# Optimization experiments

Measured on AMD Instinct MI355X. Metric: run time of the kernel, lower is better.

The kernel has to match this reference:

```python
import jax, jax.numpy as jnp
import numpy as np
import math

HEAD_DIM = 128
NUM_Q_HEAD = 32
NUM_KV_HEAD = 8
WINDOW = 512
CAP = 30.0
CLIP_LO, CLIP_HI = -0.03, 1.03
EPS = 1e-5
SCALE = 1.0 / math.sqrt(HEAD_DIM)
B, S = 2, 2048


def group_rms_norm(x, w, group_size, eps):
    # x: [B, S, hidden]; normalize each contiguous group of size group_size
    Bx, Sx, H = x.shape
    ng = H // group_size
    xg = x.reshape(Bx, Sx, ng, group_size)
    inv = jax.lax.rsqrt(jnp.mean(xg * xg, axis=-1, keepdims=True) + eps)
    return (xg * inv).reshape(Bx, Sx, H) * w


def setup_inputs() -> dict:
    key = jax.random.key(0)
    kq, kk, kv, kw1, kw2 = jax.random.split(key, 5)
    q = jax.random.normal(kq, (B, S, NUM_Q_HEAD, HEAD_DIM), dtype=jnp.float32)
    k = jax.random.normal(kk, (B, S, NUM_KV_HEAD, HEAD_DIM), dtype=jnp.float32)
    v = jax.random.normal(kv, (B, S, NUM_KV_HEAD, HEAD_DIM), dtype=jnp.float32)
    # GroupRMSNorm weights, init uniform in (-1, 1)
    q_norm_w = jax.random.uniform(kw1, (NUM_Q_HEAD * HEAD_DIM,), dtype=jnp.float32, minval=-1.0, maxval=1.0)
    kv_norm_w = jax.random.uniform(kw2, (NUM_KV_HEAD * HEAD_DIM,), dtype=jnp.float32, minval=-1.0, maxval=1.0)
    return {"q": q, "k": k, "v": v, "q_norm_w": q_norm_w, "kv_norm_w": kv_norm_w}


def reference(q, k, v, q_norm_w, kv_norm_w):
    Bq, Sq, Hq, D = q.shape
    Sk = k.shape[1]
    # QK GroupRMSNorm over flattened hidden dim, group_size = head_dim
    qn = group_rms_norm(q.reshape(Bq, Sq, Hq * D), q_norm_w, HEAD_DIM, EPS).reshape(q.shape)
    kn = group_rms_norm(k.reshape(Bq, Sk, NUM_KV_HEAD * D), kv_norm_w, HEAD_DIM, EPS).reshape(k.shape)
    # GQA: repeat_interleave kv heads along head axis
    rep = Hq // NUM_KV_HEAD
    kr = jnp.repeat(kn, rep, axis=2)  # [B, Sk, Hq, D]
    vr = jnp.repeat(v, rep, axis=2)
    # scores: [B, Hq, Sq, Sk]
    scores = jnp.einsum("bqhd,bkhd->bhqk", qn, kr) * SCALE
    scores = CAP * jnp.tanh(scores / CAP)  # softmax capping
    # sliding-window + causal mask: allowed iff i - WINDOW <= j <= i (offset = Sk - Sq = 0)
    offset = Sk - Sq
    i = jnp.arange(Sq)[:, None] + offset
    j = jnp.arange(Sk)[None, :]
    allowed = (j <= i) & (j >= i - WINDOW)
    scores = jnp.where(allowed, scores, -jnp.inf)
    probs = jax.nn.softmax(scores, axis=-1)
    probs = jnp.nan_to_num(probs, nan=0.0)
    # softmax clipping
    probs = jnp.clip((CLIP_HI - CLIP_LO) * probs + CLIP_LO, 0.0, 1.0)
    out = jnp.einsum("bhqk,bkhd->bqhd", probs, vr)
    return out
```

## Files before the change

### kernel.cpp

```cpp
#include <hip/hip_runtime.h>

#define SEQ 2048
#define DD 128
#define HQ 32
#define HKV 8
#define WIN 512

typedef unsigned short u16;
typedef unsigned int u32;
typedef __attribute__((ext_vector_type(8))) short bf16x8;
typedef __attribute__((ext_vector_type(4))) float f32x4;
typedef __attribute__((ext_vector_type(2))) float f32x2;

#define SBAR() asm volatile("s_barrier" ::: "memory")
#define WAITV0() asm volatile("s_waitcnt vmcnt(0)" ::: "memory")

__device__ __forceinline__ u16 f2bf(float f) {
  u32 u = __builtin_bit_cast(u32, f);
  u += 0x7FFFu + ((u >> 16) & 1u);
  return (u16)(u >> 16);
}

__device__ __forceinline__ void gl16(const void* g, void* l) {
  __builtin_amdgcn_global_load_lds(
      (const __attribute__((address_space(1))) void*)g,
      (__attribute__((address_space(3))) void*)l, 16, 0, 0);
}

__device__ __forceinline__ u32 cvtpk(float lo, float hi) {
  u32 r;
  asm("v_cvt_pk_bf16_f32 %0, %1, %2" : "=v"(r) : "v"(lo), "v"(hi));
  return r;
}

__device__ __forceinline__ f32x2 pk_mul(f32x2 a, f32x2 b) {
  f32x2 d;
  asm("v_pk_mul_f32 %0, %1, %2" : "=v"(d) : "v"(a), "v"(b));
  return d;
}
__device__ __forceinline__ f32x2 pk_fma(f32x2 a, f32x2 b, f32x2 c) {
  f32x2 d;
  asm("v_pk_fma_f32 %0, %1, %2, %3" : "=v"(d) : "v"(a), "v"(b), "v"(c));
  return d;
}
__device__ __forceinline__ f32x2 pk_add(f32x2 a, f32x2 b) {
  f32x2 d;
  asm("v_pk_add_f32 %0, %1, %2" : "=v"(d) : "v"(a), "v"(b));
  return d;
}

__device__ __forceinline__ f32x2 score2(f32x2 x, f32x2 vL2E, f32x2 vmCE, f32x2 vmCTL) {
  f32x2 x2 = pk_mul(x, x);
  f32x2 a1 = pk_fma(x, vL2E, vmCE);
  f32x2 b1 = pk_mul(x2, vmCTL);
  return pk_fma(b1, x, a1);
}

__device__ __forceinline__ f32x2 unpk(u32 wv) {
  f32x2 r;
  r[0] = __builtin_bit_cast(float, wv << 16);
  r[1] = __builtin_bit_cast(float, wv & 0xFFFF0000u);
  return r;
}

__device__ __forceinline__ void norm_body(
    const float* __restrict__ x, const float* __restrict__ w,
    u16* __restrict__ o, int hshift, int blk, int tid) {
  const int lane = tid & 63;
  const int wv = tid >> 6;
  const int sub = lane >> 5;
  const int l5 = lane & 31;
  const int rid = blk * 8 + wv * 2 + sub;
  const int H = 1 << hshift;
  const int hh = rid & (H - 1);
  const int s = (rid >> hshift) & (SEQ - 1);
  const int b = rid >> (hshift + 11);
  const float4 xv = *(reinterpret_cast<const float4*>(x + (size_t)rid * DD) + l5);
  float ssq = xv.x * xv.x + xv.y * xv.y + xv.z * xv.z + xv.w * xv.w;
  ssq += __shfl_xor(ssq, 1);
  ssq += __shfl_xor(ssq, 2);
  ssq += __shfl_xor(ssq, 4);
  ssq += __shfl_xor(ssq, 8);
  ssq += __shfl_xor(ssq, 16);
  const float inv = rsqrtf(ssq * (1.0f / 128.0f) + 1e-5f);
  const float4 wv4 = *(reinterpret_cast<const float4*>(w + hh * DD) + l5);
  const u16 o0 = f2bf(xv.x * inv * wv4.x);
  const u16 o1 = f2bf(xv.y * inv * wv4.y);
  const u16 o2 = f2bf(xv.z * inv * wv4.z);
  const u16 o3 = f2bf(xv.w * inv * wv4.w);
  const size_t oo = (((size_t)b * H + hh) * SEQ + s) * DD + l5 * 4;
  uint2 pk;
  pk.x = (u32)o0 | ((u32)o1 << 16);
  pk.y = (u32)o2 | ((u32)o3 << 16);
  *reinterpret_cast<uint2*>(o + oo) = pk;
}

__device__ __forceinline__ void transv_body(
    const float* __restrict__ v, u16* __restrict__ vt, int bid, int t) {
  const int st = bid & 31;
  const int h = (bid >> 5) & 7;
  const int b = bid >> 8;
  const int sbase = st * 64;
  const int d = t & 127;
  const int sch = (t >> 7) * 32;
  const size_t oo = (((size_t)(b * HKV + h)) * DD + d) * SEQ + sbase + sch;
#pragma unroll
  for (int q8 = 0; q8 < 4; ++q8) {
    uint4 o;
    u32 c[4];
#pragma unroll
    for (int p = 0; p < 4; ++p) {
      const int ss0 = q8 * 8 + p * 2;
      const int s0 = sbase + sch + ss0;
      const float a0 = v[((size_t)(b * SEQ + s0) * HKV + h) * DD + d];
      const float a1 = v[((size_t)(b * SEQ + s0 + 1) * HKV + h) * DD + d];
      c[p] = (u32)f2bf(a0) | ((u32)f2bf(a1) << 16);
    }
    o.x = c[0]; o.y = c[1]; o.z = c[2]; o.w = c[3];
    *reinterpret_cast<uint4*>(vt + oo + q8 * 8) = o;
  }
}

__global__ void __launch_bounds__(256) prep_kernel(
    const float* __restrict__ k, const float* __restrict__ v,
    const float* __restrict__ kw, u16* __restrict__ kn, u16* __restrict__ vt) {
  const int blk = blockIdx.x;
  const int tid = threadIdx.x;
  if (blk < 4096) {
    norm_body(k, kw, kn, 3, blk, tid);
  } else {
    transv_body(v, vt, blk - 4096, tid);
  }
}

__global__ void __launch_bounds__(256, 3) attn_kernel(
    const float* __restrict__ q32, const float* __restrict__ qw,
    const u16* __restrict__ kn, const u16* __restrict__ vt,
    float* __restrict__ out) {
  __shared__ char smem[32768];
  const int tid = threadIdx.x;
  const int w = tid >> 6;
  const int lane = tid & 63;
  const int c = lane & 15;
  const int g = lane >> 4;

  const int p = blockIdx.x;
  const int bid = ((p & 7) << 8) + (p >> 3);
  const int qt = (bid & 127) ^ 127;
  const int hk = (bid >> 7) & 7;
  const int b = bid >> 10;
  const int i0 = qt * 16;
  const int h = hk * 4 + w;

  const u16* kbp = kn + (size_t)(b * HKV + hk) * SEQ * DD;
  const u16* vbp = vt + (size_t)(b * HKV + hk) * DD * SEQ;

  int ks = i0 - WIN;
  ks = (ks < 0) ? 0 : (ks & ~63);
  const int ntl = (i0 + 16 - ks + 63) >> 6;

  auto stageK = [&](int kb, int bufoff) {
    char* dst = smem + bufoff;
#pragma unroll
    for (int ci = 0; ci < 4; ++ci) {
      const int call = w * 4 + ci;
      const int row = call * 4 + g;
      const int ch = c ^ (row & 7);
      gl16(kbp + (size_t)(kb + row) * DD + ch * 8, dst + call * 1024);
    }
  };
  auto stageV = [&](int kb, int bufoff) {
    char* dst = smem + bufoff;
#pragma unroll
    for (int ci = 0; ci < 4; ++ci) {
      const int call = w * 4 + ci;
      const int vrow = call * 8 + (lane >> 3);
      const int vch = (lane & 7) ^ (vrow & 7);
      gl16(vbp + (size_t)vrow * SEQ + kb + vch * 8, dst + call * 1024);
    }
  };

  stageK(ks, 0);

  union AQ { bf16x8 v; u32 w4[4]; };
  AQ aq[4];
  {
    const float* qf = q32 + (((size_t)b * SEQ + i0 + c) * HQ + h) * DD;
    const float* wf = qw + h * DD;
    float xv[4][8];
    float ss = 0.0f;
#pragma unroll
    for (int kt = 0; kt < 4; ++kt) {
      const float4 a0 = *reinterpret_cast<const float4*>(qf + kt * 32 + g * 8);
      const float4 a1 = *reinterpret_cast<const float4*>(qf + kt * 32 + g * 8 + 4);
      xv[kt][0] = a0.x; xv[kt][1] = a0.y; xv[kt][2] = a0.z; xv[kt][3] = a0.w;
      xv[kt][4] = a1.x; xv[kt][5] = a1.y; xv[kt][6] = a1.z; xv[kt][7] = a1.w;
      ss = fmaf(a0.x, a0.x, ss); ss = fmaf(a0.y, a0.y, ss);
      ss = fmaf(a0.z, a0.z, ss); ss = fmaf(a0.w, a0.w, ss);
      ss = fmaf(a1.x, a1.x, ss); ss = fmaf(a1.y, a1.y, ss);
      ss = fmaf(a1.z, a1.z, ss); ss = fmaf(a1.w, a1.w, ss);
    }
    ss += __shfl_xor(ss, 16);
    ss += __shfl_xor(ss, 32);
    const float inv = rsqrtf(ss * (1.0f / 128.0f) + 1e-5f) * 0.08838834764831845f;
#pragma unroll
    for (int kt = 0; kt < 4; ++kt) {
      const float4 w0 = *reinterpret_cast<const float4*>(wf + kt * 32 + g * 8);
      const float4 w1 = *reinterpret_cast<const float4*>(wf + kt * 32 + g * 8 + 4);
      aq[kt].w4[0] = cvtpk(xv[kt][0] * inv * w0.x, xv[kt][1] * inv * w0.y);
      aq[kt].w4[1] = cvtpk(xv[kt][2] * inv * w0.z, xv[kt][3] * inv * w0.w);
      aq[kt].w4[2] = cvtpk(xv[kt][4] * inv * w1.x, xv[kt][5] * inv * w1.y);
      aq[kt].w4[3] = cvtpk(xv[kt][6] * inv * w1.z, xv[kt][7] * inv * w1.w);
    }
  }

  const f32x2 vL2E = {1.44269504088896f, 1.44269504088896f};
  const f32x2 vmCE = {-43.2808512266689f, -43.2808512266689f};
  const f32x2 vmCTL = {-5.343315e-4f, -5.343315e-4f};

  u32 ebuf[9][8];
  f32x2 lsum2 = {0.0f, 0.0f};

#pragma unroll
  for (int t = 0; t < 9; ++t) {
    if (t >= ntl) continue;
    const int kb = ks + t * 64;
    WAITV0();
    SBAR();
    if (t + 1 < ntl) stageK(kb + 64, ((t + 1) & 1) << 14);

    const char* kbuf = smem + ((t & 1) << 14);
    f32x4 sc[4] = {};
    __builtin_amdgcn_s_setprio(1);
#pragma unroll
    for (int nt = 0; nt < 4; ++nt) {
      const int jb = kb + nt * 16;
      if (jb > i0 + 15 || jb + 15 < i0 - WIN) continue;
      const int row = nt * 16 + c;
      const int sw = row & 7;
      const char* base = kbuf + row * 256;
#pragma unroll
      for (int kt = 0; kt < 4; ++kt) {
        const bf16x8 bk = *reinterpret_cast<const bf16x8*>(base + (((kt * 4 + g) ^ sw) << 4));
        sc[nt] = __builtin_amdgcn_mfma_f32_16x16x32_bf16(bk, aq[kt].v, sc[nt], 0, 0, 0);
      }
    }
    __builtin_amdgcn_s_setprio(0);

#pragma unroll
    for (int nt = 0; nt < 4; ++nt) {
      const int jb = kb + nt * 16;
      if (jb > i0 + 15 || jb + 15 < i0 - WIN) {
        ebuf[t][nt * 2] = 0;
        ebuf[t][nt * 2 + 1] = 0;
        continue;
      }
      const bool needmask = (jb + 15 > i0) || (jb < i0 + 15 - WIN);
      f32x2 lo = __builtin_shufflevector(sc[nt], sc[nt], 0, 1);
      f32x2 hi = __builtin_shufflevector(sc[nt], sc[nt], 2, 3);
      const f32x2 a0 = score2(lo, vL2E, vmCE, vmCTL);
      const f32x2 a1 = score2(hi, vL2E, vmCE, vmCTL);
      float e0 = __builtin_amdgcn_exp2f(a0[0]);
      float e1 = __builtin_amdgcn_exp2f(a0[1]);
      float e2 = __builtin_amdgcn_exp2f(a1[0]);
      float e3 = __builtin_amdgcn_exp2f(a1[1]);
      if (needmask) {
        const int difg = i0 + c - jb - g * 4;
        e0 = ((u32)(difg - 0) <= WIN) ? e0 : 0.0f;
        e1 = ((u32)(difg - 1) <= WIN) ? e1 : 0.0f;
        e2 = ((u32)(difg - 2) <= WIN) ? e2 : 0.0f;
        e3 = ((u32)(difg - 3) <= WIN) ? e3 : 0.0f;
      }
      ebuf[t][nt * 2] = cvtpk(e0, e1);
      ebuf[t][nt * 2 + 1] = cvtpk(e2, e3);
      const f32x2 eA = {e0, e1};
      const f32x2 eB = {e2, e3};
      lsum2 = pk_add(lsum2, pk_add(eA, eB));
    }
  }
  WAITV0();
  SBAR();

  stageV(ks, 0);

  float l = lsum2[0] + lsum2[1];
  l += __shfl_xor(l, 16);
  l += __shfl_xor(l, 32);
  const float ar = 1.06f / l;
  const f32x2 var2 = {ar, ar};
  const f32x2 vm003 = {-0.03f, -0.03f};

  f32x4 acc[8] = {};

#pragma unroll
  for (int t = 0; t < 9; ++t) {
    if (t >= ntl) continue;
    const int kb = ks + t * 64;
    WAITV0();
    SBAR();
    if (t + 1 < ntl) stageV(kb + 64, ((t + 1) & 1) << 14);
    const char* ldsV = smem + ((t & 1) << 14);

#pragma unroll
    for (int k2 = 0; k2 < 2; ++k2) {
      const int jb2 = kb + k2 * 32;
      if (jb2 > i0 + 15 || jb2 + 31 < i0 - WIN) continue;

      u32 cw[4];
#pragma unroll
      for (int u = 0; u < 4; ++u) {
        const f32x2 ef = unpk(ebuf[t][k2 * 4 + u]);
        const f32x2 pr = pk_fma(ef, var2, vm003);
        cw[u] = cvtpk(__builtin_amdgcn_fmed3f(pr[0], 0.0f, 1.0f),
                      __builtin_amdgcn_fmed3f(pr[1], 0.0f, 1.0f));
      }

      union PU { bf16x8 v; u32 w4[4]; };
      PU pf;
      {
        u32 x0 = cw[0], y0 = cw[2];
        asm("v_permlane32_swap_b32 %0, %1" : "+v"(x0), "+v"(y0));
        asm("v_permlane16_swap_b32 %0, %1" : "+v"(x0), "+v"(y0));
        u32 x1 = cw[1], y1 = cw[3];
        asm("v_permlane32_swap_b32 %0, %1" : "+v"(x1), "+v"(y1));
        asm("v_permlane16_swap_b32 %0, %1" : "+v"(x1), "+v"(y1));
        pf.w4[0] = x0;
        pf.w4[1] = x1;
        pf.w4[2] = y0;
        pf.w4[3] = y1;
      }

      __builtin_amdgcn_s_setprio(1);
#pragma unroll
      for (int dt = 0; dt < 8; ++dt) {
        const int rv = dt * 16 + c;
        const bf16x8 bv = *reinterpret_cast<const bf16x8*>(
            ldsV + rv * 128 + (((k2 * 4 + g) ^ (rv & 7)) << 4));
        acc[dt] = __builtin_amdgcn_mfma_f32_16x16x32_bf16(pf.v, bv, acc[dt], 0, 0, 0);
      }
      __builtin_amdgcn_s_setprio(0);
    }
  }

#pragma unroll
  for (int r = 0; r < 4; ++r) {
    const int i = i0 + g * 4 + r;
    float* op = out + (((size_t)b * SEQ + i) * HQ + h) * DD + c;
#pragma unroll
    for (int dt = 0; dt < 8; ++dt) op[dt * 16] = acc[dt][r];
  }
}

extern "C" void kernel_launch(void* const* d_in, const int* in_sizes, int n_in,
                              void* d_out, int out_size, void* d_ws, size_t ws_size,
                              hipStream_t stream) {
  const float* q = (const float*)d_in[0];
  const float* k = (const float*)d_in[1];
  const float* v = (const float*)d_in[2];
  const float* qw = (const float*)d_in[3];
  const float* kw = (const float*)d_in[4];
  float* out = (float*)d_out;

  u16* kn = (u16*)d_ws;
  u16* vt = kn + (size_t)2 * HKV * SEQ * DD;

  prep_kernel<<<4608, 256, 0, stream>>>(k, v, kw, kn, vt);
  attn_kernel<<<2048, 256, 0, stream>>>(q, qw, kn, vt, out);
}
```

Measured before the change: 86.42 us.

## Overlap first V tile load with last K tile and hoist Q loads

Issues the first V tile's async LDS load during the final K-pass iteration, into the buffer not in use, and removes the separate wait and barrier between the QK and PV passes. V buffer parity is now offset by ntl to stay consistent. Q and norm-weight global loads are hoisted ahead of the first K staging so their latency overlaps, using nontemporal loads, and the output uses nontemporal stores. This risks buffer-parity mistakes but otherwise keeps the same work.

```diff
diff --git a/kernel.cpp b/kernel.cpp
--- a/kernel.cpp
+++ b/kernel.cpp
@@ -180,37 +180,51 @@
     }
   };
 
+  const float* qf = q32 + (((size_t)b * SEQ + i0 + c) * HQ + h) * DD;
+  const float* wf = qw + h * DD;
+  f32x4 qx[4][2];
+#pragma unroll
+  for (int kt = 0; kt < 4; ++kt) {
+    qx[kt][0] = __builtin_nontemporal_load(
+        reinterpret_cast<const f32x4*>(qf + kt * 32 + g * 8));
+    qx[kt][1] = __builtin_nontemporal_load(
+        reinterpret_cast<const f32x4*>(qf + kt * 32 + g * 8 + 4));
+  }
+  f32x4 qwv[4][2];
+#pragma unroll
+  for (int kt = 0; kt < 4; ++kt) {
+    qwv[kt][0] = *reinterpret_cast<const f32x4*>(wf + kt * 32 + g * 8);
+    qwv[kt][1] = *reinterpret_cast<const f32x4*>(wf + kt * 32 + g * 8 + 4);
+  }
+
   stageK(ks, 0);
 
   union AQ { bf16x8 v; u32 w4[4]; };
   AQ aq[4];
   {
-    const float* qf = q32 + (((size_t)b * SEQ + i0 + c) * HQ + h) * DD;
-    const float* wf = qw + h * DD;
-    float xv[4][8];
     float ss = 0.0f;
 #pragma unroll
     for (int kt = 0; kt < 4; ++kt) {
-      const float4 a0 = *reinterpret_cast<const float4*>(qf + kt * 32 + g * 8);
-      const float4 a1 = *reinterpret_cast<const float4*>(qf + kt * 32 + g * 8 + 4);
-      xv[kt][0] = a0.x; xv[kt][1] = a0.y; xv[kt][2] = a0.z; xv[kt][3] = a0.w;
-      xv[kt][4] = a1.x; xv[kt][5] = a1.y; xv[kt][6] = a1.z; xv[kt][7] = a1.w;
-      ss = fmaf(a0.x, a0.x, ss); ss = fmaf(a0.y, a0.y, ss);
-      ss = fmaf(a0.z, a0.z, ss); ss = fmaf(a0.w, a0.w, ss);
-      ss = fmaf(a1.x, a1.x, ss); ss = fmaf(a1.y, a1.y, ss);
-      ss = fmaf(a1.z, a1.z, ss); ss = fmaf(a1.w, a1.w, ss);
+#pragma unroll
+      for (int half = 0; half < 2; ++half) {
+        const f32x4 a = qx[kt][half];
+        ss = fmaf(a[0], a[0], ss); ss = fmaf(a[1], a[1], ss);
+        ss = fmaf(a[2], a[2], ss); ss = fmaf(a[3], a[3], ss);
+      }
     }
     ss += __shfl_xor(ss, 16);
     ss += __shfl_xor(ss, 32);
     const float inv = rsqrtf(ss * (1.0f / 128.0f) + 1e-5f) * 0.08838834764831845f;
 #pragma unroll
     for (int kt = 0; kt < 4; ++kt) {
-      const float4 w0 = *reinterpret_cast<const float4*>(wf + kt * 32 + g * 8);
-      const float4 w1 = *reinterpret_cast<const float4*>(wf + kt * 32 + g * 8 + 4);
-      aq[kt].w4[0] = cvtpk(xv[kt][0] * inv * w0.x, xv[kt][1] * inv * w0.y);
-      aq[kt].w4[1] = cvtpk(xv[kt][2] * inv * w0.z, xv[kt][3] * inv * w0.w);
-      aq[kt].w4[2] = cvtpk(xv[kt][4] * inv * w1.x, xv[kt][5] * inv * w1.y);
-      aq[kt].w4[3] = cvtpk(xv[kt][6] * inv * w1.z, xv[kt][7] * inv * w1.w);
+      const f32x4 a0 = qx[kt][0];
+      const f32x4 a1 = qx[kt][1];
+      const f32x4 w0 = qwv[kt][0];
+      const f32x4 w1 = qwv[kt][1];
+      aq[kt].w4[0] = cvtpk(a0[0] * inv * w0[0], a0[1] * inv * w0[1]);
+      aq[kt].w4[1] = cvtpk(a0[2] * inv * w0[2], a0[3] * inv * w0[3]);
+      aq[kt].w4[2] = cvtpk(a1[0] * inv * w1[0], a1[1] * inv * w1[1]);
+      aq[kt].w4[3] = cvtpk(a1[2] * inv * w1[2], a1[3] * inv * w1[3]);
     }
   }
 
@@ -227,7 +241,11 @@
     const int kb = ks + t * 64;
     WAITV0();
     SBAR();
-    if (t + 1 < ntl) stageK(kb + 64, ((t + 1) & 1) << 14);
+    if (t + 1 < ntl) {
+      stageK(kb + 64, ((t + 1) & 1) << 14);
+    } else {
+      stageV(ks, (ntl & 1) << 14);
+    }
 
     const char* kbuf = smem + ((t & 1) << 14);
     f32x4 sc[4] = {};
@@ -278,10 +296,6 @@
       lsum2 = pk_add(lsum2, pk_add(eA, eB));
     }
   }
-  WAITV0();
-  SBAR();
-
-  stageV(ks, 0);
 
   float l = lsum2[0] + lsum2[1];
   l += __shfl_xor(l, 16);
@@ -298,8 +312,8 @@
     const int kb = ks + t * 64;
     WAITV0();
     SBAR();
-    if (t + 1 < ntl) stageV(kb + 64, ((t + 1) & 1) << 14);
-    const char* ldsV = smem + ((t & 1) << 14);
+    if (t + 1 < ntl) stageV(kb + 64, (((t + 1) + ntl) & 1) << 14);
+    const char* ldsV = smem + (((t + ntl) & 1) << 14);
 
 #pragma unroll
     for (int k2 = 0; k2 < 2; ++k2) {
@@ -347,7 +361,8 @@
     const int i = i0 + g * 4 + r;
     float* op = out + (((size_t)b * SEQ + i) * HQ + h) * DD + c;
 #pragma unroll
-    for (int dt = 0; dt < 8; ++dt) op[dt * 16] = acc[dt][r];
+    for (int dt = 0; dt < 8; ++dt)
+      __builtin_nontemporal_store(acc[dt][r], op + dt * 16);
   }
 }
 
```

New measurement: 91.32 us. 1.06x slower.
